# Performance work log

Measured on AMD Instinct MI355X. Metric: run time of the kernel, lower is better.

The kernel has to match this reference:

```python
import jax, jax.numpy as jnp
import numpy as np

N, B, D, A, E, H = 8, 32768, 128, 64, 32, 128


def setup_inputs() -> dict:
    key = jax.random.key(0)
    ks = jax.random.split(key, 22)
    g = lambda k, shape: (jax.random.normal(k, shape, dtype=jnp.float32) * 0.1)
    return {
        "states": jax.random.normal(ks[0], (N, B, D), dtype=jnp.float32),
        # per-agent DQN (2-hidden-layer MLP), stacked over agents
        "W1": g(ks[1], (N, D, H)), "b1": g(ks[2], (N, H)),
        "W2": g(ks[3], (N, H, H)), "b2": g(ks[4], (N, H)),
        "W3": g(ks[5], (N, H, A)), "b3": g(ks[6], (N, A)),
        # per-agent query MLP
        "Wq1": g(ks[7], (N, D, E)), "bq1": g(ks[8], (N, E)),
        "Wq2": g(ks[9], (N, E, E)), "bq2": g(ks[10], (N, E)),
        # per-agent key Linear
        "Wk": g(ks[11], (N, D, E)), "bk": g(ks[12], (N, E)),
        # shared scaling MLP (D->1->1)
        "Ws1": g(ks[13], (D, 1)), "bs1": g(ks[14], (1,)),
        "Ws2": g(ks[15], (1, 1)), "bs2": g(ks[16], (1,)),
        # shared constraint MLP (D->E->1)
        "Wc1": g(ks[17], (D, E)), "bc1": g(ks[18], (E,)),
        "Wc2": g(ks[19], (E, 1)), "bc2": g(ks[20], (1,)),
    }


def reference(states, W1, b1, W2, b2, W3, b3, Wq1, bq1, Wq2, bq2, Wk, bk,
              Ws1, bs1, Ws2, bs2, Wc1, bc1, Wc2, bc2):
    relu = jax.nn.relu
    # per-agent DQN -> q_values [B, N, A]
    h = relu(jnp.einsum('nbd,ndh->nbh', states, W1) + b1[:, None, :])
    h = relu(jnp.einsum('nbh,nhk->nbk', h, W2) + b2[:, None, :])
    q_values = (jnp.einsum('nbh,nha->nba', h, W3) + b3[:, None, :]).transpose(1, 0, 2)
    # per-agent keys [B, N, E]
    keys = (jnp.einsum('nbd,nde->nbe', states, Wk) + bk[:, None, :]).transpose(1, 0, 2)
    # per-agent queries [B, N, E]
    qh = relu(jnp.einsum('nbd,nde->nbe', states, Wq1) + bq1[:, None, :])
    queries = (jnp.einsum('nbe,nef->nbf', qh, Wq2) + bq2[:, None, :]).transpose(1, 0, 2)
    # attention [B, N, N]
    scores = jnp.einsum('bnd,bmd->bnm', queries, keys) / jnp.sqrt(jnp.float32(E))
    attn = jax.nn.softmax(scores, axis=-1)
    # faithful to original einsum 'bnm,bna->bna' (sums attn over m)
    weighted_qs = jnp.einsum('bnm,bna->bna', attn, q_values)
    # shared scaling MLP, sigmoid gate [B, N, 1]
    s = relu(jnp.einsum('nbd,do->nbo', states, Ws1) + bs1)
    s = jnp.einsum('nbo,op->nbp', s, Ws2) + bs2
    scaling = jax.nn.sigmoid(s.transpose(1, 0, 2))
    summed_q = jnp.mean(scaling * weighted_qs, axis=1)  # [B, A]
    # shared constraint MLP [B, N, 1] -> mean over agents [B, 1]
    c = relu(jnp.einsum('nbd,de->nbe', states, Wc1) + bc1)
    c = (jnp.einsum('nbe,eo->nbo', c, Wc2) + bc2).transpose(1, 0, 2)
    c = jnp.mean(c, axis=1)
    return summed_q + c  # [B, A]
```

## Files before the change

kernel.cpp:

```cpp
#include <hip/hip_runtime.h>
#include <hip/hip_bf16.h>

#define NAG 8
#define BATCH 32768
#define DDIM 128
#define ADIM 64
#define HDIM 128

#define NJ1 11
#define NJ2 8
#define NJ3 4
#define FB_L1 (NJ1*4)
#define FB_L2 (NJ2*4)
#define FB_L3 (NJ3*4)
#define FB_TOT (FB_L1+FB_L2+FB_L3)
#define WAGENT (FB_TOT*512)

typedef __attribute__((ext_vector_type(8))) short bf16x8;
typedef __attribute__((ext_vector_type(4))) float f32x4;
typedef __attribute__((ext_vector_type(4))) unsigned int u32x4;

static __device__ __forceinline__ unsigned short f2bf(float f) {
  unsigned int u = __builtin_bit_cast(unsigned int, f);
  u += 0x7fffu + ((u >> 16) & 1u);
  return (unsigned short)(u >> 16);
}

__global__ void __launch_bounds__(256)
prep_weights(const float* __restrict__ W1, const float* __restrict__ W2,
             const float* __restrict__ W3, const float* __restrict__ Wc1,
             const float* __restrict__ Ws1, const float* __restrict__ b1,
             const float* __restrict__ bc1, const float* __restrict__ bs1,
             unsigned short* __restrict__ wbuf, float* __restrict__ b1e)
{
  int tid = blockIdx.x * 256 + threadIdx.x;
  if (tid < NAG * WAGENT) {
    int agent = tid / WAGENT;
    int rem   = tid % WAGENT;
    int fb = rem >> 9;
    int li = rem & 511;
    int l = li >> 3, t = li & 7;
    int lr = l & 15, lg = l >> 4;
    float v = 0.0f;
    if (fb < FB_L1) {
      int j = fb >> 2, kk = fb & 3;
      int col = j*16 + lr, k = kk*32 + lg*8 + t;
      if (col < 128)       v = W1[((size_t)agent*128 + k)*128 + col];
      else if (col < 160)  v = Wc1[k*32 + (col-128)];
      else if (col == 160) v = Ws1[k];
    } else if (fb < FB_L1 + FB_L2) {
      int f = fb - FB_L1;
      int j = f >> 2, kk = f & 3;
      int col = j*16 + lr, k = kk*32 + lg*8 + t;
      v = W2[((size_t)agent*128 + k)*128 + col];
    } else {
      int f = fb - FB_L1 - FB_L2;
      int j = f >> 2, kk = f & 3;
      int col = j*16 + lr, k = kk*32 + lg*8 + t;
      v = W3[((size_t)agent*128 + k)*64 + col];
    }
    wbuf[tid] = f2bf(v);
  }
  if (tid < NAG * 176) {
    int agent = tid / 176, col = tid % 176;
    float v = 0.0f;
    if (col < 128)       v = b1[agent*128 + col];
    else if (col < 160)  v = bc1[col - 128];
    else if (col == 160) v = bs1[0];
    b1e[tid] = v;
  }
}

__global__ void __launch_bounds__(256, 1)
qatten_main(const float* __restrict__ states,
            const float* __restrict__ b2g, const float* __restrict__ b3g,
            const float* __restrict__ ws2p, const float* __restrict__ bs2p,
            const float* __restrict__ wc2g, const float* __restrict__ bc2p,
            const unsigned short* __restrict__ wbuf,
            const float* __restrict__ b1e,
            float* __restrict__ out)
{
  __shared__ __align__(16) unsigned short wlds[WAGENT];
  __shared__ __align__(16) unsigned short hlds[4][32*128];

  const int tid  = threadIdx.x;
  const int wave = tid >> 6;
  const int lane = tid & 63;
  const int lr   = lane & 15;
  const int lg   = lane >> 4;
  const int wave_row = blockIdx.x * 128 + wave * 32;

  const float ws2  = ws2p[0];
  const float bs2v = bs2p[0];
  const float bc2v = bc2p[0];
  const float wc2a = wc2g[lr];
  const float wc2b = wc2g[16 + lr];

  const f32x4 zero4 = {0.f, 0.f, 0.f, 0.f};

  f32x4 out_acc[2][NJ3];
  float c_acc[2][4];
#pragma unroll
  for (int m = 0; m < 2; ++m) {
#pragma unroll
    for (int j = 0; j < NJ3; ++j) out_acc[m][j] = zero4;
#pragma unroll
    for (int r = 0; r < 4; ++r) c_acc[m][r] = 0.f;
  }

  unsigned short* hp = hlds[wave];

  for (int agent = 0; agent < NAG; ++agent) {
    __syncthreads();
    {
      const u32x4* wg = (const u32x4*)(wbuf + (size_t)agent * WAGENT);
      u32x4* wl = (u32x4*)wlds;
#pragma unroll
      for (int i = 0; i < 23; ++i)
        wl[i*256 + tid] = wg[i*256 + tid];
    }
    __syncthreads();

    float b1v[NJ1], b2v[NJ2], b3v[NJ3];
#pragma unroll
    for (int j = 0; j < NJ1; ++j) b1v[j] = b1e[agent*176 + j*16 + lr];
#pragma unroll
    for (int j = 0; j < NJ2; ++j) b2v[j] = b2g[agent*HDIM + j*16 + lr];
#pragma unroll
    for (int j = 0; j < NJ3; ++j) b3v[j] = b3g[agent*ADIM + j*16 + lr];

    bf16x8 afr[2][4];
    {
      const float* sb = states + ((size_t)agent * BATCH + wave_row) * DDIM;
#pragma unroll
      for (int m = 0; m < 2; ++m)
#pragma unroll
        for (int kk = 0; kk < 4; ++kk) {
          const float* p = sb + (m*16 + lr)*DDIM + kk*32 + lg*8;
          f32x4 v0 = *(const f32x4*)p;
          f32x4 v1 = *(const f32x4*)(p + 4);
          bf16x8 t;
          t[0]=(short)f2bf(v0[0]); t[1]=(short)f2bf(v0[1]);
          t[2]=(short)f2bf(v0[2]); t[3]=(short)f2bf(v0[3]);
          t[4]=(short)f2bf(v1[0]); t[5]=(short)f2bf(v1[1]);
          t[6]=(short)f2bf(v1[2]); t[7]=(short)f2bf(v1[3]);
          afr[m][kk] = t;
        }
    }

    f32x4 e_acc[2][3];
#pragma unroll
    for (int j = 0; j < NJ1; ++j) {
      bf16x8 bfr[4];
#pragma unroll
      for (int kk = 0; kk < 4; ++kk)
        bfr[kk] = *(const bf16x8*)&wlds[(j*4 + kk)*512 + lane*8];
#pragma unroll
      for (int m = 0; m < 2; ++m) {
        f32x4 acc = zero4;
#pragma unroll
        for (int kk = 0; kk < 4; ++kk)
          acc = __builtin_amdgcn_mfma_f32_16x16x32_bf16(afr[m][kk], bfr[kk], acc, 0, 0, 0);
        if (j < 8) {
#pragma unroll
          for (int r = 0; r < 4; ++r) {
            float hv = acc[r] + b1v[j];
            hv = hv > 0.f ? hv : 0.f;
            int row = m*16 + lg*4 + r;
            int bo = row*256 + (((j*16 + lr)*2) ^ ((row & 7) << 4));
            *(unsigned short*)((char*)hp + bo) = f2bf(hv);
          }
        } else {
          e_acc[m][j-8] = acc;
        }
      }
    }

    asm volatile("s_waitcnt lgkmcnt(0)" ::: "memory");
#pragma unroll
    for (int m = 0; m < 2; ++m)
#pragma unroll
      for (int kk = 0; kk < 4; ++kk) {
        int row = m*16 + lr;
        int bo = row*256 + ((kk*64 + lg*16) ^ ((row & 7) << 4));
        afr[m][kk] = *(const bf16x8*)((char*)hp + bo);
      }

#pragma unroll
    for (int j = 0; j < NJ2; ++j) {
      bf16x8 bfr[4];
#pragma unroll
      for (int kk = 0; kk < 4; ++kk)
        bfr[kk] = *(const bf16x8*)&wlds[(FB_L1 + j*4 + kk)*512 + lane*8];
#pragma unroll
      for (int m = 0; m < 2; ++m) {
        f32x4 acc = zero4;
#pragma unroll
        for (int kk = 0; kk < 4; ++kk)
          acc = __builtin_amdgcn_mfma_f32_16x16x32_bf16(afr[m][kk], bfr[kk], acc, 0, 0, 0);
#pragma unroll
        for (int r = 0; r < 4; ++r) {
          float hv = acc[r] + b2v[j];
          hv = hv > 0.f ? hv : 0.f;
          int row = m*16 + lg*4 + r;
          int bo = row*256 + (((j*16 + lr)*2) ^ ((row & 7) << 4));
          *(unsigned short*)((char*)hp + bo) = f2bf(hv);
        }
      }
    }

    asm volatile("s_waitcnt lgkmcnt(0)" ::: "memory");
#pragma unroll
    for (int m = 0; m < 2; ++m)
#pragma unroll
      for (int kk = 0; kk < 4; ++kk) {
        int row = m*16 + lr;
        int bo = row*256 + ((kk*64 + lg*16) ^ ((row & 7) << 4));
        afr[m][kk] = *(const bf16x8*)((char*)hp + bo);
      }

    float scl[2][4];
#pragma unroll
    for (int m = 0; m < 2; ++m) {
#pragma unroll
      for (int r = 0; r < 4; ++r) {
        float c0 = e_acc[m][0][r] + b1v[8];  c0 = c0 > 0.f ? c0 : 0.f;
        float c1 = e_acc[m][1][r] + b1v[9];  c1 = c1 > 0.f ? c1 : 0.f;
        float cd = c0*wc2a + c1*wc2b;
        cd += __shfl_xor(cd, 1);
        cd += __shfl_xor(cd, 2);
        cd += __shfl_xor(cd, 4);
        cd += __shfl_xor(cd, 8);
        c_acc[m][r] += cd + bc2v;
        float sp = e_acc[m][2][r] + b1v[10];
        sp = __shfl(sp, lane & 48);
        sp = sp > 0.f ? sp : 0.f;
        float s = ws2 * sp + bs2v;
        scl[m][r] = 1.f / (1.f + __expf(-s));
      }
    }

#pragma unroll
    for (int j = 0; j < NJ3; ++j) {
      bf16x8 bfr[4];
#pragma unroll
      for (int kk = 0; kk < 4; ++kk)
        bfr[kk] = *(const bf16x8*)&wlds[(FB_L1 + FB_L2 + j*4 + kk)*512 + lane*8];
#pragma unroll
      for (int m = 0; m < 2; ++m) {
        f32x4 acc = zero4;
#pragma unroll
        for (int kk = 0; kk < 4; ++kk)
          acc = __builtin_amdgcn_mfma_f32_16x16x32_bf16(afr[m][kk], bfr[kk], acc, 0, 0, 0);
#pragma unroll
        for (int r = 0; r < 4; ++r)
          out_acc[m][j][r] += scl[m][r] * (acc[r] + b3v[j]);
      }
    }
  }

#pragma unroll
  for (int m = 0; m < 2; ++m)
#pragma unroll
    for (int j = 0; j < NJ3; ++j)
#pragma unroll
      for (int r = 0; r < 4; ++r) {
        size_t row = (size_t)wave_row + m*16 + lg*4 + r;
        out[row*ADIM + j*16 + lr] = (out_acc[m][j][r] + c_acc[m][r]) * 0.125f;
      }
}

extern "C" void kernel_launch(void* const* d_in, const int* in_sizes, int n_in,
                              void* d_out, int out_size, void* d_ws, size_t ws_size,
                              hipStream_t stream)
{
  const float* states = (const float*)d_in[0];
  const float* W1  = (const float*)d_in[1];
  const float* b1  = (const float*)d_in[2];
  const float* W2  = (const float*)d_in[3];
  const float* b2  = (const float*)d_in[4];
  const float* W3  = (const float*)d_in[5];
  const float* b3  = (const float*)d_in[6];
  const float* Ws1 = (const float*)d_in[13];
  const float* bs1 = (const float*)d_in[14];
  const float* Ws2 = (const float*)d_in[15];
  const float* bs2 = (const float*)d_in[16];
  const float* Wc1 = (const float*)d_in[17];
  const float* bc1 = (const float*)d_in[18];
  const float* Wc2 = (const float*)d_in[19];
  const float* bc2 = (const float*)d_in[20];

  unsigned short* wbuf = (unsigned short*)d_ws;
  float* b1e = (float*)((char*)d_ws + (size_t)NAG * WAGENT * 2);

  dim3 pb(256), pg((NAG * WAGENT + 255) / 256);
  prep_weights<<<pg, pb, 0, stream>>>(W1, W2, W3, Wc1, Ws1, b1, bc1, bs1, wbuf, b1e);

  dim3 mb(256), mg(BATCH / 128);
  qatten_main<<<mg, mb, 0, stream>>>(states, b2, b3, Ws2, bs2, Wc2, bc2,
                                     wbuf, b1e, (float*)d_out);
}
```

Before: 73.53 us.

## Assign one agent per wave and reduce agent outputs through LDS

Each block now runs 8 waves, one per agent. Each wave reads its agent's packed bf16 weights straight from global/L2 rather than staging them into LDS with block barriers on every agent. The waves process 64 rows per pass and then sum their partial outputs across agents through LDS before writing the output. This removes the per-agent weight staging and barriers, and it adds packed bf16 conversion instructions. In exchange, B-fragments are now fetched from global memory inside the MFMA loops, the register footprint per wave grows, and a cross-wave LDS reduction is added.

```diff
diff --git a/kernel.cpp b/kernel.cpp
--- a/kernel.cpp
+++ b/kernel.cpp
@@ -24,6 +24,12 @@
   unsigned int u = __builtin_bit_cast(unsigned int, f);
   u += 0x7fffu + ((u >> 16) & 1u);
   return (unsigned short)(u >> 16);
+}
+
+static __device__ __forceinline__ unsigned int cvt_pk_bf16(float a, float b) {
+  unsigned int r;
+  asm("v_cvt_pk_bf16_f32 %0, %1, %2" : "=v"(r) : "v"(a), "v"(b));
+  return r;
 }
 
 __global__ void __launch_bounds__(256)
@@ -71,7 +77,7 @@
   }
 }
 
-__global__ void __launch_bounds__(256, 1)
+__global__ void __launch_bounds__(512, 2)
 qatten_main(const float* __restrict__ states,
             const float* __restrict__ b2g, const float* __restrict__ b3g,
             const float* __restrict__ ws2p, const float* __restrict__ bs2p,
@@ -80,16 +86,25 @@
             const float* __restrict__ b1e,
             float* __restrict__ out)
 {
-  __shared__ __align__(16) unsigned short wlds[WAGENT];
-  __shared__ __align__(16) unsigned short hlds[4][32*128];
+  __shared__ __align__(16) unsigned short hlds[8 * 8192];
 
   const int tid  = threadIdx.x;
   const int wave = tid >> 6;
   const int lane = tid & 63;
   const int lr   = lane & 15;
   const int lg   = lane >> 4;
-  const int wave_row = blockIdx.x * 128 + wave * 32;
-
+  const int agent = wave;
+
+  const unsigned short* wag = wbuf + (size_t)agent * WAGENT;
+  unsigned short* hp = hlds + wave * 8192;
+
+  float b1v[NJ1], b2v[NJ2], b3v[NJ3];
+#pragma unroll
+  for (int j = 0; j < NJ1; ++j) b1v[j] = b1e[agent*176 + j*16 + lr];
+#pragma unroll
+  for (int j = 0; j < NJ2; ++j) b2v[j] = b2g[agent*HDIM + j*16 + lr];
+#pragma unroll
+  for (int j = 0; j < NJ3; ++j) b3v[j] = b3g[agent*ADIM + j*16 + lr];
   const float ws2  = ws2p[0];
   const float bs2v = bs2p[0];
   const float bc2v = bc2p[0];
@@ -98,87 +113,93 @@
 
   const f32x4 zero4 = {0.f, 0.f, 0.f, 0.f};
 
-  f32x4 out_acc[2][NJ3];
-  float c_acc[2][4];
-#pragma unroll
-  for (int m = 0; m < 2; ++m) {
-#pragma unroll
-    for (int j = 0; j < NJ3; ++j) out_acc[m][j] = zero4;
-#pragma unroll
-    for (int r = 0; r < 4; ++r) c_acc[m][r] = 0.f;
-  }
-
-  unsigned short* hp = hlds[wave];
-
-  for (int agent = 0; agent < NAG; ++agent) {
-    __syncthreads();
+  for (int pass = 0; pass < 2; ++pass) {
+    const int row0 = blockIdx.x * 128 + pass * 64;
+
+    bf16x8 afr[4][4];
     {
-      const u32x4* wg = (const u32x4*)(wbuf + (size_t)agent * WAGENT);
-      u32x4* wl = (u32x4*)wlds;
-#pragma unroll
-      for (int i = 0; i < 23; ++i)
-        wl[i*256 + tid] = wg[i*256 + tid];
-    }
-    __syncthreads();
-
-    float b1v[NJ1], b2v[NJ2], b3v[NJ3];
-#pragma unroll
-    for (int j = 0; j < NJ1; ++j) b1v[j] = b1e[agent*176 + j*16 + lr];
-#pragma unroll
-    for (int j = 0; j < NJ2; ++j) b2v[j] = b2g[agent*HDIM + j*16 + lr];
-#pragma unroll
-    for (int j = 0; j < NJ3; ++j) b3v[j] = b3g[agent*ADIM + j*16 + lr];
-
-    bf16x8 afr[2][4];
-    {
-      const float* sb = states + ((size_t)agent * BATCH + wave_row) * DDIM;
-#pragma unroll
-      for (int m = 0; m < 2; ++m)
+      const float* sb = states + ((size_t)agent * BATCH + row0) * DDIM;
+#pragma unroll
+      for (int m = 0; m < 4; ++m)
 #pragma unroll
         for (int kk = 0; kk < 4; ++kk) {
           const float* p = sb + (m*16 + lr)*DDIM + kk*32 + lg*8;
           f32x4 v0 = *(const f32x4*)p;
           f32x4 v1 = *(const f32x4*)(p + 4);
-          bf16x8 t;
-          t[0]=(short)f2bf(v0[0]); t[1]=(short)f2bf(v0[1]);
-          t[2]=(short)f2bf(v0[2]); t[3]=(short)f2bf(v0[3]);
-          t[4]=(short)f2bf(v1[0]); t[5]=(short)f2bf(v1[1]);
-          t[6]=(short)f2bf(v1[2]); t[7]=(short)f2bf(v1[3]);
-          afr[m][kk] = t;
-        }
-    }
-
-    f32x4 e_acc[2][3];
-#pragma unroll
-    for (int j = 0; j < NJ1; ++j) {
+          u32x4 w;
+          w[0] = cvt_pk_bf16(v0[0], v0[1]);
+          w[1] = cvt_pk_bf16(v0[2], v0[3]);
+          w[2] = cvt_pk_bf16(v1[0], v1[1]);
+          w[3] = cvt_pk_bf16(v1[2], v1[3]);
+          afr[m][kk] = __builtin_bit_cast(bf16x8, w);
+        }
+    }
+
+    float scl[4][4], crow[4][4];
+    {
+      f32x4 eacc[3][4];
+#pragma unroll
+      for (int jx = 0; jx < 3; ++jx) {
+        bf16x8 bfr[4];
+#pragma unroll
+        for (int kk = 0; kk < 4; ++kk)
+          bfr[kk] = *(const bf16x8*)&wag[((8+jx)*4 + kk)*512 + lane*8];
+#pragma unroll
+        for (int m = 0; m < 4; ++m) {
+          f32x4 a = zero4;
+#pragma unroll
+          for (int kk = 0; kk < 4; ++kk)
+            a = __builtin_amdgcn_mfma_f32_16x16x32_bf16(afr[m][kk], bfr[kk], a, 0, 0, 0);
+          eacc[jx][m] = a;
+        }
+      }
+#pragma unroll
+      for (int m = 0; m < 4; ++m) {
+#pragma unroll
+        for (int r = 0; r < 4; ++r) {
+          float c0 = eacc[0][m][r] + b1v[8];  c0 = c0 > 0.f ? c0 : 0.f;
+          float c1 = eacc[1][m][r] + b1v[9];  c1 = c1 > 0.f ? c1 : 0.f;
+          float cd = c0*wc2a + c1*wc2b;
+          cd += __shfl_xor(cd, 1);
+          cd += __shfl_xor(cd, 2);
+          cd += __shfl_xor(cd, 4);
+          cd += __shfl_xor(cd, 8);
+          crow[m][r] = cd + bc2v;
+          float sp = eacc[2][m][r] + b1v[10];
+          sp = __shfl(sp, lane & 48);
+          sp = sp > 0.f ? sp : 0.f;
+          float s = ws2 * sp + bs2v;
+          scl[m][r] = 1.f / (1.f + __expf(-s));
+        }
+      }
+    }
+
+#pragma unroll
+    for (int j = 0; j < 8; ++j) {
       bf16x8 bfr[4];
 #pragma unroll
       for (int kk = 0; kk < 4; ++kk)
-        bfr[kk] = *(const bf16x8*)&wlds[(j*4 + kk)*512 + lane*8];
-#pragma unroll
-      for (int m = 0; m < 2; ++m) {
+        bfr[kk] = *(const bf16x8*)&wag[(j*4 + kk)*512 + lane*8];
+#pragma unroll
+      for (int m = 0; m < 4; ++m) {
         f32x4 acc = zero4;
 #pragma unroll
         for (int kk = 0; kk < 4; ++kk)
           acc = __builtin_amdgcn_mfma_f32_16x16x32_bf16(afr[m][kk], bfr[kk], acc, 0, 0, 0);
-        if (j < 8) {
-#pragma unroll
-          for (int r = 0; r < 4; ++r) {
-            float hv = acc[r] + b1v[j];
-            hv = hv > 0.f ? hv : 0.f;
-            int row = m*16 + lg*4 + r;
-            int bo = row*256 + (((j*16 + lr)*2) ^ ((row & 7) << 4));
-            *(unsigned short*)((char*)hp + bo) = f2bf(hv);
-          }
-        } else {
-          e_acc[m][j-8] = acc;
+#pragma unroll
+        for (int r = 0; r < 4; ++r) {
+          float hv = acc[r] + b1v[j];
+          hv = hv > 0.f ? hv : 0.f;
+          int row = m*16 + lg*4 + r;
+          int bo = row*256 + (((j*16 + lr)*2) ^ ((row & 7) << 4));
+          *(unsigned short*)((char*)hp + bo) = f2bf(hv);
         }
       }
     }
 
     asm volatile("s_waitcnt lgkmcnt(0)" ::: "memory");
 #pragma unroll
-    for (int m = 0; m < 2; ++m)
+    for (int m = 0; m < 4; ++m)
 #pragma unroll
       for (int kk = 0; kk < 4; ++kk) {
         int row = m*16 + lr;
@@ -187,13 +208,13 @@
       }
 
 #pragma unroll
-    for (int j = 0; j < NJ2; ++j) {
+    for (int j = 0; j < 8; ++j) {
       bf16x8 bfr[4];
 #pragma unroll
       for (int kk = 0; kk < 4; ++kk)
-        bfr[kk] = *(const bf16x8*)&wlds[(FB_L1 + j*4 + kk)*512 + lane*8];
-#pragma unroll
-      for (int m = 0; m < 2; ++m) {
+        bfr[kk] = *(const bf16x8*)&wag[(FB_L1 + j*4 + kk)*512 + lane*8];
+#pragma unroll
+      for (int m = 0; m < 4; ++m) {
         f32x4 acc = zero4;
 #pragma unroll
         for (int kk = 0; kk < 4; ++kk)
@@ -211,7 +232,7 @@
 
     asm volatile("s_waitcnt lgkmcnt(0)" ::: "memory");
 #pragma unroll
-    for (int m = 0; m < 2; ++m)
+    for (int m = 0; m < 4; ++m)
 #pragma unroll
       for (int kk = 0; kk < 4; ++kk) {
         int row = m*16 + lr;
@@ -219,55 +240,55 @@
         afr[m][kk] = *(const bf16x8*)((char*)hp + bo);
       }
 
-    float scl[2][4];
-#pragma unroll
-    for (int m = 0; m < 2; ++m) {
-#pragma unroll
-      for (int r = 0; r < 4; ++r) {
-        float c0 = e_acc[m][0][r] + b1v[8];  c0 = c0 > 0.f ? c0 : 0.f;
-        float c1 = e_acc[m][1][r] + b1v[9];  c1 = c1 > 0.f ? c1 : 0.f;
-        float cd = c0*wc2a + c1*wc2b;
-        cd += __shfl_xor(cd, 1);
-        cd += __shfl_xor(cd, 2);
-        cd += __shfl_xor(cd, 4);
-        cd += __shfl_xor(cd, 8);
-        c_acc[m][r] += cd + bc2v;
-        float sp = e_acc[m][2][r] + b1v[10];
-        sp = __shfl(sp, lane & 48);
-        sp = sp > 0.f ? sp : 0.f;
-        float s = ws2 * sp + bs2v;
-        scl[m][r] = 1.f / (1.f + __expf(-s));
-      }
-    }
-
+    f32x4 out_acc[4][NJ3];
 #pragma unroll
     for (int j = 0; j < NJ3; ++j) {
       bf16x8 bfr[4];
 #pragma unroll
       for (int kk = 0; kk < 4; ++kk)
-        bfr[kk] = *(const bf16x8*)&wlds[(FB_L1 + FB_L2 + j*4 + kk)*512 + lane*8];
-#pragma unroll
-      for (int m = 0; m < 2; ++m) {
+        bfr[kk] = *(const bf16x8*)&wag[(FB_L1 + FB_L2 + j*4 + kk)*512 + lane*8];
+#pragma unroll
+      for (int m = 0; m < 4; ++m) {
         f32x4 acc = zero4;
 #pragma unroll
         for (int kk = 0; kk < 4; ++kk)
           acc = __builtin_amdgcn_mfma_f32_16x16x32_bf16(afr[m][kk], bfr[kk], acc, 0, 0, 0);
 #pragma unroll
         for (int r = 0; r < 4; ++r)
-          out_acc[m][j][r] += scl[m][r] * (acc[r] + b3v[j]);
-      }
-    }
+          out_acc[m][j][r] = scl[m][r] * (acc[r] + b3v[j]) + crow[m][r];
+      }
+    }
+
+    asm volatile("s_waitcnt lgkmcnt(0)" ::: "memory");
+#pragma unroll
+    for (int m = 0; m < 4; ++m)
+#pragma unroll
+      for (int j = 0; j < NJ3; ++j)
+        *(f32x4*)&hp[((m*4 + j)*64 + lane)*8] = out_acc[m][j];
+
+    __syncthreads();
+
+#pragma unroll
+    for (int s2 = 0; s2 < 2; ++s2) {
+      int s = tid + s2*512;
+      f32x4 sum = zero4;
+#pragma unroll
+      for (int w = 0; w < 8; ++w) {
+        f32x4 v = *(const f32x4*)&hlds[(w*8192) + s*8];
+        sum[0] += v[0]; sum[1] += v[1]; sum[2] += v[2]; sum[3] += v[3];
+      }
+      int mj = s >> 6, ln = s & 63;
+      int m = mj >> 2, j = mj & 3;
+      int lg2 = ln >> 4, lr2 = ln & 15;
+#pragma unroll
+      for (int r = 0; r < 4; ++r) {
+        int row = row0 + m*16 + lg2*4 + r;
+        out[(size_t)row*ADIM + j*16 + lr2] = sum[r] * 0.125f;
+      }
+    }
+
+    __syncthreads();
   }
-
-#pragma unroll
-  for (int m = 0; m < 2; ++m)
-#pragma unroll
-    for (int j = 0; j < NJ3; ++j)
-#pragma unroll
-      for (int r = 0; r < 4; ++r) {
-        size_t row = (size_t)wave_row + m*16 + lg*4 + r;
-        out[row*ADIM + j*16 + lr] = (out_acc[m][j][r] + c_acc[m][r]) * 0.125f;
-      }
 }
 
 extern "C" void kernel_launch(void* const* d_in, const int* in_sizes, int n_in,
@@ -296,7 +317,7 @@
   dim3 pb(256), pg((NAG * WAGENT + 255) / 256);
   prep_weights<<<pg, pb, 0, stream>>>(W1, W2, W3, Wc1, Ws1, b1, bc1, bs1, wbuf, b1e);
 
-  dim3 mb(256), mg(BATCH / 128);
+  dim3 mb(512), mg(BATCH / 128);
   qatten_main<<<mg, mb, 0, stream>>>(states, b2, b3, Ws2, bs2, Wc2, bc2,
                                      wbuf, b1e, (float*)d_out);
 }
```

Result: slower. 166.5 us (+126.4%).
